# Kernel tuning notes

Hardware: AMD Instinct MI355X
Metric: run time of the kernel (lower is better)

## Reference

```python
import jax, jax.numpy as jnp
import numpy as np

N_MIN = 16
N_TABLES = 16
PER_LEVEL_SCALE = 1.3195079565048218
MAX_TABLE = 2 ** 19
H1, H2, H3 = 1, 2654435761, 805459861
OFFS = np.array([[0,0,0],[0,0,1],[0,1,0],[0,1,1],[1,0,0],[1,0,1],[1,1,0],[1,1,1]], dtype=np.int32)

def _levels():
    N_l, sizes, max_direct = [], [], 0
    for i in range(N_TABLES):
        res = int(np.ceil(N_MIN * np.exp(i * np.log(PER_LEVEL_SCALE)) - 1.0)) + 1
        ts = res ** 3
        ts = ts if ts % 8 == 0 else ((ts + 7) // 8) * 8
        ts = min(MAX_TABLE, ts)
        if ts == res ** 3:
            max_direct = i
        N_l.append(res); sizes.append(ts)
    return N_l, sizes, max_direct

N_L, SIZES, MAX_DIRECT = _levels()

def hash_encode(pos, grids):
    # pos: [N,3] in [0,1); grids: [16, MAX_TABLE, 2] (levels padded to MAX_TABLE)
    feats = []
    for l in range(N_TABLES):
        uvz = pos * jnp.float32(N_L[l])
        iuv_f = jnp.floor(uvz)
        f = uvz - iuv_f                                   # fractional part [N,3]
        corners = iuv_f.astype(jnp.int32)[:, None, :] + OFFS[None]  # [N,8,3]
        if l <= MAX_DIRECT:
            R = N_L[l]
            idx = (corners[..., 2] * (R * R) + corners[..., 1] * R + corners[..., 0]) % SIZES[l]
        else:
            cu = corners.astype(jnp.uint32)
            h = (cu[..., 0] * jnp.uint32(H1)) ^ (cu[..., 1] * jnp.uint32(H2)) ^ (cu[..., 2] * jnp.uint32(H3))
            idx = (h % jnp.uint32(SIZES[l])).astype(jnp.int32)
        c = grids[l][idx]                                 # gather -> [N,8,2]
        fx, fy, fz = f[:, 0:1], f[:, 1:2], f[:, 2:3]
        c00 = c[:, 0] * (1 - fx) + c[:, 4] * fx
        c01 = c[:, 1] * (1 - fx) + c[:, 5] * fx
        c10 = c[:, 2] * (1 - fx) + c[:, 6] * fx
        c11 = c[:, 3] * (1 - fx) + c[:, 7] * fx
        c0 = c00 * (1 - fy) + c10 * fy
        c1 = c01 * (1 - fy) + c11 * fy
        feats.append(c0 * (1 - fz) + c1 * fy)  # NOTE: c1*fy (not fz) replicates source exactly
    return jnp.concatenate(feats, axis=-1)  # [N, 32]

def setup_inputs():
    key = jax.random.key(0)
    ks = jax.random.split(key, 7)
    N = 1048576  # max_samples(512) * batch_size(2048)
    x = jax.random.uniform(ks[0], (N, 19), dtype=jnp.float32)  # pos(3) in [0,1) + dir feats(16)
    grids = (jax.random.uniform(ks[1], (N_TABLES, MAX_TABLE, 2), dtype=jnp.float32) * 2.0 - 1.0) * 1e-4
    h = 64
    w_sigma1 = jax.random.normal(ks[2], (32, h), dtype=jnp.float32) / np.sqrt(32).astype(np.float32)
    w_sigma2 = jax.random.normal(ks[3], (h, 16), dtype=jnp.float32) / np.sqrt(h).astype(np.float32)
    w_c1 = jax.random.normal(ks[4], (32, h), dtype=jnp.float32) / np.sqrt(32).astype(np.float32)
    w_c2 = jax.random.normal(ks[5], (h, h), dtype=jnp.float32) / np.sqrt(h).astype(np.float32)
    w_c3 = jax.random.normal(ks[6], (h, 3), dtype=jnp.float32) / np.sqrt(h).astype(np.float32)
    return {"x": x, "grids": grids, "w_sigma1": w_sigma1, "w_sigma2": w_sigma2,
            "w_c1": w_c1, "w_c2": w_c2, "w_c3": w_c3}

def reference(x, grids, w_sigma1, w_sigma2, w_c1, w_c2, w_c3):
    pos, direc = x[:, :3], x[:, 3:]
    enc = hash_encode(pos, grids)                       # [N,32]
    out = jax.nn.relu(enc @ w_sigma1) @ w_sigma2        # [N,16]
    sigma = out[:, 0]
    ci = jnp.concatenate([direc, out], axis=-1)         # [N,32]
    color = jax.nn.sigmoid(jax.nn.relu(jax.nn.relu(ci @ w_c1) @ w_c2) @ w_c3)  # [N,3]
    return jnp.concatenate([color, sigma[:, None]], axis=-1)  # [N,4]
```

## Files before the change

kernel.cpp:

```cpp
#include <hip/hip_runtime.h>
#include <math.h>


#define BLOCK 256
#define NTAB  (16*524288)
#define PITCH 88

constexpr int      kNL[16] = {16,22,28,37,49,65,85,112,148,195,257,338,446,589,777,1025};
constexpr unsigned kSZ[16] = {4096u,10648u,21952u,50656u,117656u,274632u,
                              524288u,524288u,524288u,524288u,524288u,
                              524288u,524288u,524288u,524288u,524288u};

typedef __attribute__((ext_vector_type(8))) short short8;
typedef __attribute__((ext_vector_type(4))) float float4v;

__device__ __forceinline__ short f2bf(float f) {
    unsigned u = __float_as_uint(f);
    unsigned r = u + 0x7fffu + ((u >> 16) & 1u);
    return (short)(r >> 16);
}
__device__ __forceinline__ float bf2f(short h) {
    return __uint_as_float(((unsigned)(unsigned short)h) << 16);
}
__device__ __forceinline__ unsigned pk2(float a, float b) {
    return ((unsigned)(unsigned short)f2bf(b) << 16) | (unsigned)(unsigned short)f2bf(a);
}
__device__ __forceinline__ float pe0(unsigned u) { return __uint_as_float(u << 16); }
__device__ __forceinline__ float pe1(unsigned u) { return __uint_as_float(u & 0xffff0000u); }

__device__ __forceinline__ unsigned trilerp_pack(const unsigned* vv, float fx, float fy, float fz)
{
    const float w0x = 1.f-fx, w0y = 1.f-fy, w0z = 1.f-fz;
    float e0, e1;
    {
        float c00 = pe0(vv[0])*w0x + pe0(vv[4])*fx;
        float c01 = pe0(vv[1])*w0x + pe0(vv[5])*fx;
        float c10 = pe0(vv[2])*w0x + pe0(vv[6])*fx;
        float c11 = pe0(vv[3])*w0x + pe0(vv[7])*fx;
        float c0 = c00*w0y + c10*fy;
        float c1 = c01*w0y + c11*fy;
        e0 = c0*w0z + c1*fy;
    }
    {
        float c00 = pe1(vv[0])*w0x + pe1(vv[4])*fx;
        float c01 = pe1(vv[1])*w0x + pe1(vv[5])*fx;
        float c10 = pe1(vv[2])*w0x + pe1(vv[6])*fx;
        float c11 = pe1(vv[3])*w0x + pe1(vv[7])*fx;
        float c0 = c00*w0y + c10*fy;
        float c1 = c01*w0y + c11*fy;
        e1 = c0*w0z + c1*fy;
    }
    return pk2(e0, e1);
}

__global__ void pack_pos(const float* __restrict__ x, float4* __restrict__ pos4, int n)
{
    int i = blockIdx.x * BLOCK + threadIdx.x;
    if (i >= n) return;
    const float* xr = x + (size_t)i * 19;
    pos4[i] = make_float4(xr[0], xr[1], xr[2], 0.f);
}

__global__ void conv_tables(const float* __restrict__ grids, unsigned* __restrict__ tbu)
{
    int i = blockIdx.x * BLOCK + threadIdx.x;
    if (i >= NTAB) return;
    float2 v = ((const float2*)grids)[i];
    tbu[i] = pk2(v.x, v.y);
}

__global__ void pack_wfrag(const float* __restrict__ w1, const float* __restrict__ w2,
                           const float* __restrict__ wc1, const float* __restrict__ wc2,
                           const float* __restrict__ wc3, uint4* __restrict__ wf)
{
    int lane = threadIdx.x;
    if (lane >= 64) return;
    int cn = lane & 15, q = lane >> 4;

    auto pack8 = [](const float* src, int stride) -> uint4 {
        uint4 r;
        r.x = pk2(src[0*stride], src[1*stride]);
        r.y = pk2(src[2*stride], src[3*stride]);
        r.z = pk2(src[4*stride], src[5*stride]);
        r.w = pk2(src[6*stride], src[7*stride]);
        return r;
    };

    int f = 0;
    for (int nt = 0; nt < 4; ++nt)
        wf[(f++)*64 + lane] = pack8(w1 + (q*8)*64 + nt*16 + cn, 64);
    for (int c = 0; c < 2; ++c)
        wf[(f++)*64 + lane] = pack8(w2 + (c*32 + q*8)*16 + cn, 16);
    for (int nt = 0; nt < 4; ++nt)
        wf[(f++)*64 + lane] = pack8(wc1 + (q*8)*64 + nt*16 + cn, 64);
    for (int c = 0; c < 2; ++c)
        for (int nt = 0; nt < 4; ++nt)
            wf[(f++)*64 + lane] = pack8(wc2 + (c*32 + q*8)*64 + nt*16 + cn, 64);
    for (int c = 0; c < 2; ++c) {
        if (cn < 3) wf[(f++)*64 + lane] = pack8(wc3 + (c*32 + q*8)*3 + cn, 3);
        else { uint4 z; z.x = z.y = z.z = z.w = 0u; wf[(f++)*64 + lane] = z; }
    }
}

template<int L>
__device__ __forceinline__ void gather4(const float4* __restrict__ pos4,
                                        const unsigned* __restrict__ tball,
                                        unsigned* __restrict__ encu,
                                        int n, int p0, int cnt)
{
    constexpr int R = kNL[L];
    constexpr unsigned S = kSZ[L];
    constexpr unsigned H2c = 2654435761u, H3c = 805459861u;
    const unsigned* __restrict__ tbu = tball + (size_t)L * 524288u;

    unsigned vv[4][8];
    float fxa[4], fya[4], fza[4];
    #pragma unroll
    for (int q = 0; q < 4; ++q) {
        if (q >= cnt) continue;
        float4 p = pos4[p0+q];
        const float Rf = (float)R;
        float ux = p.x*Rf, uy = p.y*Rf, uz = p.z*Rf;
        float gx = floorf(ux), gy = floorf(uy), gz = floorf(uz);
        fxa[q] = ux-gx; fya[q] = uy-gy; fza[q] = uz-gz;
        int ix = (int)gx, iy = (int)gy, iz = (int)gz;

        if (L >= 6) {
            unsigned tc[4];
            #pragma unroll
            for (int c = 0; c < 4; ++c) {
                int yb = c >> 1, zb = c & 1;
                tc[c] = (unsigned)(iy+yb)*H2c ^ (unsigned)(iz+zb)*H3c;
            }
            if ((ix & 1) == 0) {
                #pragma unroll
                for (int c = 0; c < 4; ++c) {
                    unsigned idx0 = ((unsigned)ix ^ tc[c]) & (S-1u);
                    uint2 pr = *(const uint2*)(tbu + (idx0 & ~1u));
                    unsigned swp = idx0 & 1u;
                    vv[q][c]   = swp ? pr.y : pr.x;
                    vv[q][4+c] = swp ? pr.x : pr.y;
                }
            } else {
                #pragma unroll
                for (int c = 0; c < 4; ++c) {
                    unsigned idx0 = ((unsigned)ix     ^ tc[c]) & (S-1u);
                    unsigned idx1 = ((unsigned)(ix+1) ^ tc[c]) & (S-1u);
                    vv[q][c]   = tbu[idx0];
                    vv[q][4+c] = tbu[idx1];
                }
            }
        } else if (L >= 3) {
            unsigned tc[4];
            #pragma unroll
            for (int c = 0; c < 4; ++c) {
                int yb = c >> 1, zb = c & 1;
                tc[c] = (unsigned)(iy+yb)*H2c ^ (unsigned)(iz+zb)*H3c;
            }
            if ((ix & 1) == 0) {
                #pragma unroll
                for (int c = 0; c < 4; ++c) {
                    unsigned h0 = (unsigned)ix ^ tc[c];
                    unsigned base = (h0 & ~1u) % S;
                    uint2 pr = *(const uint2*)(tbu + base);
                    unsigned swp = h0 & 1u;
                    vv[q][c]   = swp ? pr.y : pr.x;
                    vv[q][4+c] = swp ? pr.x : pr.y;
                }
            } else {
                #pragma unroll
                for (int c = 0; c < 4; ++c) {
                    unsigned h0 = ((unsigned)ix)     ^ tc[c];
                    unsigned h1 = ((unsigned)(ix+1)) ^ tc[c];
                    vv[q][c]   = tbu[h0 % S];
                    vv[q][4+c] = tbu[h1 % S];
                }
            }
        } else {
            #pragma unroll
            for (int j = 0; j < 8; ++j) {
                int ox = ix + ((j>>2)&1);
                int oy = iy + ((j>>1)&1);
                int oz = iz + (j&1);
                vv[q][j] = tbu[(unsigned)((oz*(R*R) + oy*R + ox) % (int)S)];
            }
        }
    }

    unsigned pkd[4];
    #pragma unroll
    for (int q = 0; q < 4; ++q) {
        if (q >= cnt) continue;
        pkd[q] = trilerp_pack(vv[q], fxa[q], fya[q], fza[q]);
    }

    unsigned* d = encu + (size_t)L*n + p0;
    if (cnt == 4) {
        uint4 o; o.x = pkd[0]; o.y = pkd[1]; o.z = pkd[2]; o.w = pkd[3];
        *(uint4*)d = o;
    } else {
        for (int q = 0; q < cnt; ++q) d[q] = pkd[q];
    }
}

__global__ __launch_bounds__(BLOCK)
void enc_all(const float4* __restrict__ pos4, const unsigned* __restrict__ tball,
             unsigned* __restrict__ encu, int n, int byA, int byB)
{
    const int bx = blockIdx.x;
    const int by = blockIdx.y;

    if (by < byA) {
        int p0 = (by*BLOCK + threadIdx.x) * 4;
        if (p0 >= n) return;
        int cnt = min(4, n - p0);
        switch (bx) {
            case 0: gather4< 6>(pos4,tball,encu,n,p0,cnt); break;
            case 1: gather4< 7>(pos4,tball,encu,n,p0,cnt); break;
            case 2: gather4< 8>(pos4,tball,encu,n,p0,cnt); break;
            case 3: gather4< 9>(pos4,tball,encu,n,p0,cnt); break;
            case 4: gather4<10>(pos4,tball,encu,n,p0,cnt); break;
            case 5: gather4<11>(pos4,tball,encu,n,p0,cnt); break;
            case 6: gather4<12>(pos4,tball,encu,n,p0,cnt); break;
            case 7: gather4<13>(pos4,tball,encu,n,p0,cnt); break;
        }
    } else if (by < byA + byB) {
        int q4 = (n + 3) / 4;
        int quarter = bx & 3;
        int jb = quarter * q4;
        int je = min(n, jb + q4);
        int p0 = jb + ((by-byA)*BLOCK + threadIdx.x) * 4;
        if (p0 >= je) return;
        int cnt = min(4, je - p0);
        if (bx < 4) gather4<14>(pos4,tball,encu,n,p0,cnt);
        else        gather4<15>(pos4,tball,encu,n,p0,cnt);
    } else {
        int cj = (by - byA - byB)*8 + bx;
        if (cj >= 3*byA) return;
        int level = cj % 3;
        int chunk = cj / 3;
        int p0 = (chunk*BLOCK + threadIdx.x) * 4;
        if (p0 >= n) return;
        int cnt = min(4, n - p0);
        switch (level) {
            case 0: gather4<3>(pos4,tball,encu,n,p0,cnt); break;
            case 1: gather4<4>(pos4,tball,encu,n,p0,cnt); break;
            case 2: gather4<5>(pos4,tball,encu,n,p0,cnt); break;
        }
    }
}

template<int LV>
__device__ __forceinline__ unsigned enc_low_t(float4 p, const unsigned* __restrict__ tball)
{
    constexpr int R = kNL[LV];
    constexpr unsigned S = kSZ[LV];
    const unsigned* __restrict__ tb = tball + (size_t)LV * 524288u;
    const float Rf = (float)R;
    float ux = p.x*Rf, uy = p.y*Rf, uz = p.z*Rf;
    float gx = floorf(ux), gy = floorf(uy), gz = floorf(uz);
    float fx = ux-gx, fy = uy-gy, fz = uz-gz;
    int ix = (int)gx, iy = (int)gy, iz = (int)gz;
    unsigned vv[8];
    #pragma unroll
    for (int j = 0; j < 8; ++j) {
        int ox = ix + ((j>>2)&1);
        int oy = iy + ((j>>1)&1);
        int oz = iz + (j&1);
        vv[j] = tb[(unsigned)((oz*(R*R) + oy*R + ox) % (int)S)];
    }
    return trilerp_pack(vv, fx, fy, fz);
}

__device__ __forceinline__ short8 ldfrag(const uint4* __restrict__ wf, int f, int lane) {
    union { uint4 u; short8 s; } cv;
    cv.u = wf[f*64 + lane];
    return cv.s;
}

__global__ __launch_bounds__(BLOCK)
void mlp_mfma(const float* __restrict__ x,
              const float4* __restrict__ pos4,
              const unsigned* __restrict__ tbu,
              const unsigned* __restrict__ encu,
              const uint4* __restrict__ wf,
              float* __restrict__ out, int n)
{
    __shared__ unsigned short s_scr[4][2][16*PITCH];
    __shared__ float s_sig[4][16];
    __shared__ float s_col[4][16][4];
    __shared__ float s_dir[4][304];
    __shared__ unsigned s_low[4][3][16];

    const int t = threadIdx.x;
    const int lane = t & 63;
    const int wave = t >> 6;
    const int m = lane & 15;
    const int q = lane >> 4;
    const int cn = m;
    const int blk = blockIdx.x * 64;
    const int pt  = blk + wave*16 + m;
    const int ptc = pt < n ? pt : n - 1;
    const int p0w = blk + wave*16;

    const float4v zero = {0.f, 0.f, 0.f, 0.f};

    {
        int npts = n - p0w; if (npts > 16) npts = 16; if (npts < 0) npts = 0;
        int nfl = npts * 19;
        const float* xs = x + (size_t)p0w * 19;
        float* sd = s_dir[wave];
        #pragma unroll
        for (int it = 0; it < 5; ++it) {
            int idx = it*64 + lane;
            if (idx < nfl) sd[idx] = xs[idx];
        }
    }

    if (lane < 48) {
        int lv = lane >> 4, pm = lane & 15;
        int pp = p0w + pm; if (pp >= n) pp = n - 1;
        float4 p = pos4[pp];
        unsigned r;
        if (lv == 0)      r = enc_low_t<0>(p, tbu);
        else if (lv == 1) r = enc_low_t<1>(p, tbu);
        else              r = enc_low_t<2>(p, tbu);
        s_low[wave][lv][pm] = r;
    }

    union { unsigned u[4]; short8 s; } a1;
    if (q == 0) {
        a1.u[0] = s_low[wave][0][m];
        a1.u[1] = s_low[wave][1][m];
        a1.u[2] = s_low[wave][2][m];
        a1.u[3] = encu[(size_t)3*n + ptc];
    } else {
        #pragma unroll
        for (int i = 0; i < 4; ++i)
            a1.u[i] = encu[(size_t)(q*4 + i)*n + ptc];
    }

    short8 bw1[4], bw2[2], bwc1[4];
    #pragma unroll
    for (int nt = 0; nt < 4; ++nt) bw1[nt] = ldfrag(wf, nt, lane);
    #pragma unroll
    for (int c = 0; c < 2; ++c)    bw2[c]  = ldfrag(wf, 4 + c, lane);
    #pragma unroll
    for (int nt = 0; nt < 4; ++nt) bwc1[nt] = ldfrag(wf, 6 + nt, lane);

    float4v h[4];
    #pragma unroll
    for (int nt = 0; nt < 4; ++nt) {
        h[nt] = __builtin_amdgcn_mfma_f32_16x16x32_bf16(a1.s, bw1[nt], zero, 0, 0, 0);
        #pragma unroll
        for (int r = 0; r < 4; ++r) h[nt][r] = fmaxf(h[nt][r], 0.f);
    }

    unsigned short* sA = &s_scr[wave][0][0];
    unsigned short* sB = &s_scr[wave][1][0];
    #pragma unroll
    for (int nt = 0; nt < 4; ++nt)
        #pragma unroll
        for (int r = 0; r < 4; ++r)
            sA[(q*4+r)*PITCH + nt*16 + cn] = (unsigned short)f2bf(h[nt][r]);
    short8 ah[2];
    #pragma unroll
    for (int c = 0; c < 2; ++c)
        ah[c] = *(const short8*)&sA[m*PITCH + c*32 + q*8];

    float4v o = __builtin_amdgcn_mfma_f32_16x16x32_bf16(ah[0], bw2[0], zero, 0, 0, 0);
    o = __builtin_amdgcn_mfma_f32_16x16x32_bf16(ah[1], bw2[1], o, 0, 0, 0);
    if (cn == 0) {
        #pragma unroll
        for (int r = 0; r < 4; ++r) s_sig[wave][q*4+r] = o[r];
    }

    #pragma unroll
    for (int r = 0; r < 4; ++r)
        sB[(q*4+r)*PITCH + cn] = (unsigned short)f2bf(o[r]);
    short8 ov = *(const short8*)&sB[m*PITCH + (q >= 2 ? (q-2)*8 : 0)];

    union { unsigned u[4]; short8 s; } ci_hi, ci_lo;
    if (q < 2) {
        const float* sd = s_dir[wave];
        int rm = ptc - p0w; if (rm < 0) rm = 0;
        #pragma unroll
        for (int i = 0; i < 4; ++i) {
            float d0 = sd[rm*19 + 3 + q*8 + 2*i];
            float d1 = sd[rm*19 + 3 + q*8 + 2*i + 1];
            short h0 = f2bf(d0), h1 = f2bf(d1);
            ci_hi.u[i] = ((unsigned)(unsigned short)h1 << 16) | (unsigned)(unsigned short)h0;
            short l0 = f2bf(d0 - bf2f(h0)), l1 = f2bf(d1 - bf2f(h1));
            ci_lo.u[i] = ((unsigned)(unsigned short)l1 << 16) | (unsigned)(unsigned short)l0;
        }
    } else {
        ci_hi.s = ov;
        #pragma unroll
        for (int i = 0; i < 4; ++i) ci_lo.u[i] = 0u;
    }

    float4v hc[4];
    #pragma unroll
    for (int nt = 0; nt < 4; ++nt) {
        hc[nt] = __builtin_amdgcn_mfma_f32_16x16x32_bf16(ci_hi.s, bwc1[nt], zero, 0, 0, 0);
        hc[nt] = __builtin_amdgcn_mfma_f32_16x16x32_bf16(ci_lo.s, bwc1[nt], hc[nt], 0, 0, 0);
        #pragma unroll
        for (int r = 0; r < 4; ++r) hc[nt][r] = fmaxf(hc[nt][r], 0.f);
    }

    short8 bwc2[2][4], bwc3[2];
    #pragma unroll
    for (int c = 0; c < 2; ++c)
        #pragma unroll
        for (int nt = 0; nt < 4; ++nt)
            bwc2[c][nt] = ldfrag(wf, 10 + c*4 + nt, lane);
    #pragma unroll
    for (int c = 0; c < 2; ++c) bwc3[c] = ldfrag(wf, 18 + c, lane);

    #pragma unroll
    for (int nt = 0; nt < 4; ++nt)
        #pragma unroll
        for (int r = 0; r < 4; ++r) {
            float v = hc[nt][r];
            short hi = f2bf(v);
            sA[(q*4+r)*PITCH + nt*16 + cn] = (unsigned short)hi;
            sB[(q*4+r)*PITCH + nt*16 + cn] = (unsigned short)f2bf(v - bf2f(hi));
        }
    short8 ghi[2], glo[2];
    #pragma unroll
    for (int c = 0; c < 2; ++c) {
        ghi[c] = *(const short8*)&sA[m*PITCH + c*32 + q*8];
        glo[c] = *(const short8*)&sB[m*PITCH + c*32 + q*8];
    }

    float4v g[4];
    #pragma unroll
    for (int nt = 0; nt < 4; ++nt) {
        float4v acc = __builtin_amdgcn_mfma_f32_16x16x32_bf16(ghi[0], bwc2[0][nt], zero, 0, 0, 0);
        acc = __builtin_amdgcn_mfma_f32_16x16x32_bf16(glo[0], bwc2[0][nt], acc, 0, 0, 0);
        acc = __builtin_amdgcn_mfma_f32_16x16x32_bf16(ghi[1], bwc2[1][nt], acc, 0, 0, 0);
        acc = __builtin_amdgcn_mfma_f32_16x16x32_bf16(glo[1], bwc2[1][nt], acc, 0, 0, 0);
        #pragma unroll
        for (int r = 0; r < 4; ++r) acc[r] = fmaxf(acc[r], 0.f);
        g[nt] = acc;
    }

    #pragma unroll
    for (int nt = 0; nt < 4; ++nt)
        #pragma unroll
        for (int r = 0; r < 4; ++r) {
            float v = g[nt][r];
            short hi = f2bf(v);
            sA[(q*4+r)*PITCH + nt*16 + cn] = (unsigned short)hi;
            sB[(q*4+r)*PITCH + nt*16 + cn] = (unsigned short)f2bf(v - bf2f(hi));
        }
    short8 uhi[2], ulo[2];
    #pragma unroll
    for (int c = 0; c < 2; ++c) {
        uhi[c] = *(const short8*)&sA[m*PITCH + c*32 + q*8];
        ulo[c] = *(const short8*)&sB[m*PITCH + c*32 + q*8];
    }

    float4v col = __builtin_amdgcn_mfma_f32_16x16x32_bf16(uhi[0], bwc3[0], zero, 0, 0, 0);
    col = __builtin_amdgcn_mfma_f32_16x16x32_bf16(ulo[0], bwc3[0], col, 0, 0, 0);
    col = __builtin_amdgcn_mfma_f32_16x16x32_bf16(uhi[1], bwc3[1], col, 0, 0, 0);
    col = __builtin_amdgcn_mfma_f32_16x16x32_bf16(ulo[1], bwc3[1], col, 0, 0, 0);
    #pragma unroll
    for (int r = 0; r < 4; ++r)
        col[r] = 1.f / (1.f + __expf(-col[r]));

    if (cn < 3) {
        #pragma unroll
        for (int r = 0; r < 4; ++r) s_col[wave][q*4+r][cn] = col[r];
    }

    __builtin_amdgcn_s_waitcnt(0);
    int pfi = lane >> 2, c4 = lane & 3;
    int pout = blk + wave*16 + pfi;
    if (pout < n) {
        float v = (c4 == 3) ? s_sig[wave][pfi] : s_col[wave][pfi][c4];
        out[(size_t)pout*4 + c4] = v;
    }
}

extern "C" void kernel_launch(void* const* d_in, const int* in_sizes, int n_in,
                              void* d_out, int out_size, void* d_ws, size_t ws_size,
                              hipStream_t stream) {
    const float* x     = (const float*)d_in[0];
    const float* grids = (const float*)d_in[1];
    const float* w1    = (const float*)d_in[2];
    const float* w2    = (const float*)d_in[3];
    const float* wc1   = (const float*)d_in[4];
    const float* wc2   = (const float*)d_in[5];
    const float* wc3   = (const float*)d_in[6];
    float* out = (float*)d_out;

    int n = in_sizes[0] / 19;
    size_t encB = (size_t)16 * n * sizeof(unsigned);
    size_t posB = (size_t)n * sizeof(float4);
    size_t tabB = (size_t)NTAB * sizeof(unsigned);

    char* p = (char*)d_ws;
    unsigned* encu = (unsigned*)p;
    float4*   pos4 = (float4*)(p + encB);
    unsigned* tbu  = (unsigned*)(p + encB + posB);
    uint4*    wf   = (uint4*)(p + encB + posB + tabB);

    pack_pos<<<(n + BLOCK - 1) / BLOCK, BLOCK, 0, stream>>>(x, pos4, n);
    conv_tables<<<(NTAB + BLOCK - 1) / BLOCK, BLOCK, 0, stream>>>(grids, tbu);
    pack_wfrag<<<1, 64, 0, stream>>>(w1, w2, wc1, wc2, wc3, wf);

    int byA = (n + BLOCK*4 - 1) / (BLOCK*4);
    int q4  = (n + 3) / 4;
    int byB = (q4 + BLOCK*4 - 1) / (BLOCK*4);
    int jobsC = 3 * byA;
    int byC = (jobsC + 7) / 8;
    dim3 ge(8, byA + byB + byC);
    enc_all<<<ge, BLOCK, 0, stream>>>(pos4, tbu, encu, n, byA, byB);

    mlp_mfma<<<(n + 63) / 64, BLOCK, 0, stream>>>(x, pos4, tbu, encu, wf, out, n);
}
```

Measured before the change: 563.5 us.

## Move hash-grid levels 3-5 encoding from gather kernel into MLP kernel

Levels 3, 4 and 5 are now encoded directly inside the MLP kernel, where lanes compute the trilinear interpolation into shared memory, instead of being written to the intermediate encoding buffer by the gather kernel. This removes the global write and re-read of three encoding planes and shrinks the gather grid. The gather template is simplified to only the power-of-two hashed path for levels 6 and up. The cost is extra divergent, latency-bound table lookups inside the MLP kernel, with lanes 0-31 doing two lookups each.

New measurement: 554.3 us. Within noise of the previous version (-1.6%).

```diff
diff --git a/kernel.cpp b/kernel.cpp
--- a/kernel.cpp
+++ b/kernel.cpp
@@ -125,64 +125,28 @@
         fxa[q] = ux-gx; fya[q] = uy-gy; fza[q] = uz-gz;
         int ix = (int)gx, iy = (int)gy, iz = (int)gz;
 
-        if (L >= 6) {
-            unsigned tc[4];
+        unsigned tc[4];
+        #pragma unroll
+        for (int c = 0; c < 4; ++c) {
+            int yb = c >> 1, zb = c & 1;
+            tc[c] = (unsigned)(iy+yb)*H2c ^ (unsigned)(iz+zb)*H3c;
+        }
+        if ((ix & 1) == 0) {
             #pragma unroll
             for (int c = 0; c < 4; ++c) {
-                int yb = c >> 1, zb = c & 1;
-                tc[c] = (unsigned)(iy+yb)*H2c ^ (unsigned)(iz+zb)*H3c;
-            }
-            if ((ix & 1) == 0) {
-                #pragma unroll
-                for (int c = 0; c < 4; ++c) {
-                    unsigned idx0 = ((unsigned)ix ^ tc[c]) & (S-1u);
-                    uint2 pr = *(const uint2*)(tbu + (idx0 & ~1u));
-                    unsigned swp = idx0 & 1u;
-                    vv[q][c]   = swp ? pr.y : pr.x;
-                    vv[q][4+c] = swp ? pr.x : pr.y;
-                }
-            } else {
-                #pragma unroll
-                for (int c = 0; c < 4; ++c) {
-                    unsigned idx0 = ((unsigned)ix     ^ tc[c]) & (S-1u);
-                    unsigned idx1 = ((unsigned)(ix+1) ^ tc[c]) & (S-1u);
-                    vv[q][c]   = tbu[idx0];
-                    vv[q][4+c] = tbu[idx1];
-                }
-            }
-        } else if (L >= 3) {
-            unsigned tc[4];
-            #pragma unroll
-            for (int c = 0; c < 4; ++c) {
-                int yb = c >> 1, zb = c & 1;
-                tc[c] = (unsigned)(iy+yb)*H2c ^ (unsigned)(iz+zb)*H3c;
-            }
-            if ((ix & 1) == 0) {
-                #pragma unroll
-                for (int c = 0; c < 4; ++c) {
-                    unsigned h0 = (unsigned)ix ^ tc[c];
-                    unsigned base = (h0 & ~1u) % S;
-                    uint2 pr = *(const uint2*)(tbu + base);
-                    unsigned swp = h0 & 1u;
-                    vv[q][c]   = swp ? pr.y : pr.x;
-                    vv[q][4+c] = swp ? pr.x : pr.y;
-                }
-            } else {
-                #pragma unroll
-                for (int c = 0; c < 4; ++c) {
-                    unsigned h0 = ((unsigned)ix)     ^ tc[c];
-                    unsigned h1 = ((unsigned)(ix+1)) ^ tc[c];
-                    vv[q][c]   = tbu[h0 % S];
-                    vv[q][4+c] = tbu[h1 % S];
-                }
+                unsigned idx0 = ((unsigned)ix ^ tc[c]) & (S-1u);
+                uint2 pr = *(const uint2*)(tbu + (idx0 & ~1u));
+                unsigned swp = idx0 & 1u;
+                vv[q][c]   = swp ? pr.y : pr.x;
+                vv[q][4+c] = swp ? pr.x : pr.y;
             }
         } else {
             #pragma unroll
-            for (int j = 0; j < 8; ++j) {
-                int ox = ix + ((j>>2)&1);
-                int oy = iy + ((j>>1)&1);
-                int oz = iz + (j&1);
-                vv[q][j] = tbu[(unsigned)((oz*(R*R) + oy*R + ox) % (int)S)];
+            for (int c = 0; c < 4; ++c) {
+                unsigned idx0 = ((unsigned)ix     ^ tc[c]) & (S-1u);
+                unsigned idx1 = ((unsigned)(ix+1) ^ tc[c]) & (S-1u);
+                vv[q][c]   = tbu[idx0];
+                vv[q][4+c] = tbu[idx1];
             }
         }
     }
@@ -205,7 +169,7 @@
 
 __global__ __launch_bounds__(BLOCK)
 void enc_all(const float4* __restrict__ pos4, const unsigned* __restrict__ tball,
-             unsigned* __restrict__ encu, int n, int byA, int byB)
+             unsigned* __restrict__ encu, int n, int byA)
 {
     const int bx = blockIdx.x;
     const int by = blockIdx.y;
@@ -224,7 +188,7 @@
             case 6: gather4<12>(pos4,tball,encu,n,p0,cnt); break;
             case 7: gather4<13>(pos4,tball,encu,n,p0,cnt); break;
         }
-    } else if (by < byA + byB) {
+    } else {
         int q4 = (n + 3) / 4;
         int quarter = bx & 3;
         int jb = quarter * q4;
@@ -234,42 +198,56 @@
         int cnt = min(4, je - p0);
         if (bx < 4) gather4<14>(pos4,tball,encu,n,p0,cnt);
         else        gather4<15>(pos4,tball,encu,n,p0,cnt);
-    } else {
-        int cj = (by - byA - byB)*8 + bx;
-        if (cj >= 3*byA) return;
-        int level = cj % 3;
-        int chunk = cj / 3;
-        int p0 = (chunk*BLOCK + threadIdx.x) * 4;
-        if (p0 >= n) return;
-        int cnt = min(4, n - p0);
-        switch (level) {
-            case 0: gather4<3>(pos4,tball,encu,n,p0,cnt); break;
-            case 1: gather4<4>(pos4,tball,encu,n,p0,cnt); break;
-            case 2: gather4<5>(pos4,tball,encu,n,p0,cnt); break;
-        }
     }
 }
 
 template<int LV>
-__device__ __forceinline__ unsigned enc_low_t(float4 p, const unsigned* __restrict__ tball)
+__device__ __forceinline__ void enc_addr(float4 p, const unsigned* __restrict__ tball,
+                                         unsigned vv[8], float& fx, float& fy, float& fz)
 {
     constexpr int R = kNL[LV];
     constexpr unsigned S = kSZ[LV];
+    constexpr unsigned H2c = 2654435761u, H3c = 805459861u;
     const unsigned* __restrict__ tb = tball + (size_t)LV * 524288u;
     const float Rf = (float)R;
     float ux = p.x*Rf, uy = p.y*Rf, uz = p.z*Rf;
     float gx = floorf(ux), gy = floorf(uy), gz = floorf(uz);
-    float fx = ux-gx, fy = uy-gy, fz = uz-gz;
+    fx = ux-gx; fy = uy-gy; fz = uz-gz;
     int ix = (int)gx, iy = (int)gy, iz = (int)gz;
-    unsigned vv[8];
-    #pragma unroll
-    for (int j = 0; j < 8; ++j) {
-        int ox = ix + ((j>>2)&1);
-        int oy = iy + ((j>>1)&1);
-        int oz = iz + (j&1);
-        vv[j] = tb[(unsigned)((oz*(R*R) + oy*R + ox) % (int)S)];
-    }
-    return trilerp_pack(vv, fx, fy, fz);
+
+    if (LV >= 3) {
+        unsigned tc[4];
+        #pragma unroll
+        for (int c = 0; c < 4; ++c) {
+            int yb = c >> 1, zb = c & 1;
+            tc[c] = (unsigned)(iy+yb)*H2c ^ (unsigned)(iz+zb)*H3c;
+        }
+        if ((ix & 1) == 0) {
+            #pragma unroll
+            for (int c = 0; c < 4; ++c) {
+                unsigned h0 = (unsigned)ix ^ tc[c];
+                unsigned base = (h0 & ~1u) % S;
+                uint2 pr = *(const uint2*)(tb + base);
+                unsigned swp = h0 & 1u;
+                vv[c]   = swp ? pr.y : pr.x;
+                vv[4+c] = swp ? pr.x : pr.y;
+            }
+        } else {
+            #pragma unroll
+            for (int c = 0; c < 4; ++c) {
+                vv[c]   = tb[(((unsigned)ix)     ^ tc[c]) % S];
+                vv[4+c] = tb[(((unsigned)(ix+1)) ^ tc[c]) % S];
+            }
+        }
+    } else {
+        #pragma unroll
+        for (int j = 0; j < 8; ++j) {
+            int ox = ix + ((j>>2)&1);
+            int oy = iy + ((j>>1)&1);
+            int oz = iz + (j&1);
+            vv[j] = tb[(unsigned)((oz*(R*R) + oy*R + ox) % (int)S)];
+        }
+    }
 }
 
 __device__ __forceinline__ short8 ldfrag(const uint4* __restrict__ wf, int f, int lane) {
@@ -290,7 +268,7 @@
     __shared__ float s_sig[4][16];
     __shared__ float s_col[4][16][4];
     __shared__ float s_dir[4][304];
-    __shared__ unsigned s_low[4][3][16];
+    __shared__ unsigned s_low[4][6][16];
 
     const int t = threadIdx.x;
     const int lane = t & 63;
@@ -317,27 +295,35 @@
         }
     }
 
-    if (lane < 48) {
+    {
         int lv = lane >> 4, pm = lane & 15;
         int pp = p0w + pm; if (pp >= n) pp = n - 1;
         float4 p = pos4[pp];
-        unsigned r;
-        if (lv == 0)      r = enc_low_t<0>(p, tbu);
-        else if (lv == 1) r = enc_low_t<1>(p, tbu);
-        else              r = enc_low_t<2>(p, tbu);
-        s_low[wave][lv][pm] = r;
+        unsigned vv[8]; float fx, fy, fz;
+        switch (lv) {
+            case 0: enc_addr<0>(p, tbu, vv, fx, fy, fz); break;
+            case 1: enc_addr<1>(p, tbu, vv, fx, fy, fz); break;
+            case 2: enc_addr<2>(p, tbu, vv, fx, fy, fz); break;
+            default: enc_addr<3>(p, tbu, vv, fx, fy, fz); break;
+        }
+        s_low[wave][lv][pm] = trilerp_pack(vv, fx, fy, fz);
+    }
+    if (lane < 32) {
+        int lv = 4 + (lane >> 4), pm = lane & 15;
+        int pp = p0w + pm; if (pp >= n) pp = n - 1;
+        float4 p = pos4[pp];
+        unsigned vv[8]; float fx, fy, fz;
+        if (lv == 4) enc_addr<4>(p, tbu, vv, fx, fy, fz);
+        else         enc_addr<5>(p, tbu, vv, fx, fy, fz);
+        s_low[wave][lv][pm] = trilerp_pack(vv, fx, fy, fz);
     }
 
     union { unsigned u[4]; short8 s; } a1;
-    if (q == 0) {
-        a1.u[0] = s_low[wave][0][m];
-        a1.u[1] = s_low[wave][1][m];
-        a1.u[2] = s_low[wave][2][m];
-        a1.u[3] = encu[(size_t)3*n + ptc];
-    } else {
-        #pragma unroll
-        for (int i = 0; i < 4; ++i)
-            a1.u[i] = encu[(size_t)(q*4 + i)*n + ptc];
+    #pragma unroll
+    for (int i = 0; i < 4; ++i) {
+        int lv = q*4 + i;
+        if (lv < 6) a1.u[i] = s_low[wave][lv][m];
+        else        a1.u[i] = encu[(size_t)lv*n + ptc];
     }
 
     short8 bw1[4], bw2[2], bwc1[4];
@@ -513,10 +499,8 @@
     int byA = (n + BLOCK*4 - 1) / (BLOCK*4);
     int q4  = (n + 3) / 4;
     int byB = (q4 + BLOCK*4 - 1) / (BLOCK*4);
-    int jobsC = 3 * byA;
-    int byC = (jobsC + 7) / 8;
-    dim3 ge(8, byA + byB + byC);
-    enc_all<<<ge, BLOCK, 0, stream>>>(pos4, tbu, encu, n, byA, byB);
+    dim3 ge(8, byA + byB);
+    enc_all<<<ge, BLOCK, 0, stream>>>(pos4, tbu, encu, n, byA);
 
     mlp_mfma<<<(n + 63) / 64, BLOCK, 0, stream>>>(x, pos4, tbu, encu, wf, out, n);
 }
```
